# Kernel optimization log

Hardware: AMD Instinct MI355X
Metric: run time of the kernel (lower is better)

The kernel has to match this reference:

```python
import jax, jax.numpy as jnp
import numpy as np

N, H, O, E, K = 131072, 128, 128, 8, 2


def setup_inputs() -> dict:
    key = jax.random.key(0)
    k1, k2, k3, k4 = jax.random.split(key, 4)
    x = jax.random.normal(k1, (N, H), dtype=jnp.float32)
    w_gate = jax.random.normal(k2, (H, E), dtype=jnp.float32) * 0.02
    w_noise = jax.random.normal(k3, (H, E), dtype=jnp.float32) * 0.02
    w_expert = jax.random.normal(k4, (E, H, O), dtype=jnp.float32) * (1.0 / np.sqrt(H))
    b_expert = jnp.zeros((E, O), dtype=jnp.float32)
    return {"x": x, "w_gate": w_gate, "w_noise": w_noise,
            "w_expert": w_expert, "b_expert": b_expert, "top_k": K}


def _gates(x, w_gate, top_k):
    # Noisy top-k gating (eval mode: noise term w_noise is inactive).
    logits = x @ w_gate                              # [N, E]
    top_vals, top_idx = jax.lax.top_k(logits, top_k)  # [N, K]
    top_gates = jax.nn.softmax(top_vals, axis=-1)     # renormalize over top-k
    n = logits.shape[0]
    rows = jnp.arange(n)[:, None]                     # [N, 1]
    gates = jnp.zeros_like(logits).at[rows, top_idx].set(top_gates)  # [N, E] sparse
    return gates


def reference(x, w_gate, w_noise, w_expert, b_expert, top_k):
    gates = _gates(x, w_gate, top_k)                                  # [N, E]
    # Dense (mathematically identical) dispatch/combine: every expert FFN
    # applied per token, weighted by its (mostly-zero) gate.
    expert_out = jnp.einsum('nh,eho->neo', x, w_expert) + b_expert     # [N, E, O]
    out = jnp.einsum('ne,neo->no', gates, expert_out)                  # [N, O]
    return out
```

## Files before the change

### kernel.cpp

```cpp
#include <hip/hip_runtime.h>
#include <math.h>

typedef __bf16 bf16x8 __attribute__((ext_vector_type(8)));
typedef float f32x16 __attribute__((ext_vector_type(16)));

#define NTOK 131072
#define HDIM 128
#define ODIM 128
#define NEXP 8

__device__ __forceinline__ unsigned short f2bf(float f){
  union { float f; unsigned u; } v; v.f = f;
  unsigned r = v.u + 0x7FFFu + ((v.u >> 16) & 1u);
  return (unsigned short)(r >> 16);
}

__global__ void pack_w(const float* __restrict__ we, unsigned short* __restrict__ pw){
  int f = blockIdx.x * 256 + threadIdx.x;
  int l   = f & 63;
  int kt2 = (f >> 6) & 3;
  int e   = (f >> 8) & 7;
  int h   = (f >> 11) & 1;
  int ot  = (f >> 12) & 3;
  int o = ot * 32 + (l & 31);
  int kbase = (h * 4 + kt2) * 16 + ((l >> 5) << 3);
  unsigned short vals[8];
#pragma unroll
  for (int j = 0; j < 8; ++j)
    vals[j] = f2bf(we[(e * HDIM + kbase + j) * ODIM + o]);
  *(bf16x8*)(pw + (size_t)f * 8) = *(bf16x8*)vals;
}

__global__ void gating_pack(const float* __restrict__ x, const float* __restrict__ wg,
                            float* __restrict__ gates_t, unsigned short* __restrict__ xf){
  __shared__ float xs[64 * 128];
  __shared__ float wgl[128 * 8];
  __shared__ float plg[64 * 36];
  int t = threadIdx.x;
  size_t tokbase = (size_t)blockIdx.x * 64;

  ((float4*)wgl)[t] = ((const float4*)wg)[t];
  {
    const float4* xsrc = (const float4*)(x + tokbase * HDIM);
#pragma unroll
    for (int i = 0; i < 8; ++i){
      int idx = i * 256 + t;
      int tok = idx >> 5, c = idx & 31;
      *(float4*)&xs[tok * 128 + ((c ^ (tok & 7)) << 2)] = xsrc[idx];
    }
  }
  __syncthreads();

  {
    int tok = t & 63, q = t >> 6;
    float lg[8];
#pragma unroll
    for (int e = 0; e < 8; ++e) lg[e] = 0.0f;
#pragma unroll
    for (int i = 0; i < 8; ++i){
      int c = q * 8 + i;
      float4 v = *(float4*)&xs[tok * 128 + ((c ^ (tok & 7)) << 2)];
      const float* wr = wgl + c * 32;
#pragma unroll
      for (int e = 0; e < 8; ++e)
        lg[e] += v.x * wr[e] + v.y * wr[8 + e] + v.z * wr[16 + e] + v.w * wr[24 + e];
    }
    *(float4*)&plg[tok * 36 + q * 8]     = make_float4(lg[0], lg[1], lg[2], lg[3]);
    *(float4*)&plg[tok * 36 + q * 8 + 4] = make_float4(lg[4], lg[5], lg[6], lg[7]);
  }
  __syncthreads();

  if (t < 64){
    float lg[8];
#pragma unroll
    for (int e = 0; e < 8; ++e)
      lg[e] = plg[t * 36 + e] + plg[t * 36 + 8 + e] + plg[t * 36 + 16 + e] + plg[t * 36 + 24 + e];
    int i1 = 0; float v1 = lg[0];
#pragma unroll
    for (int e = 1; e < 8; ++e) if (lg[e] > v1){ v1 = lg[e]; i1 = e; }
    int i2 = -1; float v2 = -3.4e38f;
#pragma unroll
    for (int e = 0; e < 8; ++e) if (e != i1 && lg[e] > v2){ v2 = lg[e]; i2 = e; }
    float ex = __expf(v2 - v1);
    float inv = 1.0f / (1.0f + ex);
#pragma unroll
    for (int e = 0; e < 8; ++e)
      gates_t[(size_t)e * NTOK + tokbase + t] = (e == i1) ? inv : ((e == i2) ? ex * inv : 0.0f);
  }

  {
    int tokL = t >> 2, q = t & 3;
    float4 cv[8];
#pragma unroll
    for (int i = 0; i < 8; ++i)
      cv[i] = *(float4*)&xs[tokL * 128 + (((q * 8 + i) ^ (tokL & 7)) << 2)];
    size_t tgG = (size_t)blockIdx.x * 2 + (tokL >> 5);
#pragma unroll
    for (int jb = 0; jb < 4; ++jb){
      int h0 = q * 32 + jb * 8;
      int kt = h0 >> 4;
      int lslot = (tokL & 31) + 32 * (jb & 1);
      float4 a = cv[2 * jb], b = cv[2 * jb + 1];
      unsigned long long lo = (unsigned long long)f2bf(a.x)
                            | ((unsigned long long)f2bf(a.y) << 16)
                            | ((unsigned long long)f2bf(a.z) << 32)
                            | ((unsigned long long)f2bf(a.w) << 48);
      unsigned long long hi = (unsigned long long)f2bf(b.x)
                            | ((unsigned long long)f2bf(b.y) << 16)
                            | ((unsigned long long)f2bf(b.z) << 32)
                            | ((unsigned long long)f2bf(b.w) << 48);
      unsigned long long* dst = (unsigned long long*)(xf + ((tgG * 8 + kt) * 64 + lslot) * 8);
      dst[0] = lo; dst[1] = hi;
    }
  }
}

__launch_bounds__(256, 2)
__global__ void moe_gemm(const unsigned short* __restrict__ pw,
                         const unsigned short* __restrict__ xf,
                         const float* __restrict__ gates_t,
                         const float* __restrict__ be, float* __restrict__ out){
  __shared__ unsigned short Wh[16384];
  __shared__ float glds[8 * 512];
  __shared__ float blds[256];

  int t = threadIdx.x;
  int ot = blockIdx.x & 3;
  int tb = blockIdx.x >> 2;
  int w = t >> 6, l = t & 63, l32 = l & 31, lh = l >> 5;
  size_t tokb = (size_t)tb * 512;

#pragma unroll
  for (int it = 0; it < 4; ++it){
    int idx = it * 256 + t;
    int e = idx >> 7, c = idx & 127;
    *(float4*)&glds[e * 512 + c * 4] =
      *(const float4*)&gates_t[(size_t)e * NTOK + tokb + c * 4];
  }
  blds[t] = be[(t >> 5) * ODIM + ot * 32 + (t & 31)];

  f32x16 zero16;
#pragma unroll
  for (int i = 0; i < 16; ++i) zero16[i] = 0.0f;
  f32x16 tot0 = zero16, tot1 = zero16, tot2 = zero16, tot3 = zero16;

#pragma unroll 1
  for (int h = 0; h < 2; ++h){
    {
      const uint4* wsrc = (const uint4*)(pw + (size_t)(ot * 2 + h) * 16384);
      uint4* wdst = (uint4*)Wh;
#pragma unroll
      for (int it = 0; it < 8; ++it)
        wdst[it * 256 + t] = wsrc[it * 256 + t];
    }
    bf16x8 xb[4][4];
#pragma unroll
    for (int tg = 0; tg < 4; ++tg){
      size_t tgG = tokb / 32 + w * 4 + tg;
#pragma unroll
      for (int kt = 0; kt < 4; ++kt)
        xb[tg][kt] = *(const bf16x8*)(xf + ((tgG * 8 + h * 4 + kt) * 64 + l) * 8);
    }
    __syncthreads();

#pragma unroll 1
    for (int e = 0; e < 8; ++e){
      float g0 = glds[e * 512 + (w * 4 + 0) * 32 + l32];
      float g1 = glds[e * 512 + (w * 4 + 1) * 32 + l32];
      float g2 = glds[e * 512 + (w * 4 + 2) * 32 + l32];
      float g3 = glds[e * 512 + (w * 4 + 3) * 32 + l32];
      {
        f32x16 p0 = zero16, p1 = zero16;
#pragma unroll
        for (int kt = 0; kt < 4; ++kt){
          bf16x8 a = *(const bf16x8*)&Wh[((e * 4 + kt) * 64 + l) * 8];
          p0 = __builtin_amdgcn_mfma_f32_32x32x16_bf16(a, xb[0][kt], p0, 0, 0, 0);
          p1 = __builtin_amdgcn_mfma_f32_32x32x16_bf16(a, xb[1][kt], p1, 0, 0, 0);
        }
#pragma unroll
        for (int r = 0; r < 16; ++r){ tot0[r] += g0 * p0[r]; tot1[r] += g1 * p1[r]; }
      }
      {
        f32x16 p0 = zero16, p1 = zero16;
#pragma unroll
        for (int kt = 0; kt < 4; ++kt){
          bf16x8 a = *(const bf16x8*)&Wh[((e * 4 + kt) * 64 + l) * 8];
          p0 = __builtin_amdgcn_mfma_f32_32x32x16_bf16(a, xb[2][kt], p0, 0, 0, 0);
          p1 = __builtin_amdgcn_mfma_f32_32x32x16_bf16(a, xb[3][kt], p1, 0, 0, 0);
        }
#pragma unroll
        for (int r = 0; r < 16; ++r){ tot2[r] += g2 * p0[r]; tot3[r] += g3 * p1[r]; }
      }
    }
    __syncthreads();
  }

#pragma unroll
  for (int e = 0; e < 8; ++e){
    float bb[16];
#pragma unroll
    for (int rg = 0; rg < 4; ++rg){
      float4 b4 = *(float4*)&blds[e * 32 + rg * 8 + lh * 4];
      bb[rg * 4 + 0] = b4.x; bb[rg * 4 + 1] = b4.y; bb[rg * 4 + 2] = b4.z; bb[rg * 4 + 3] = b4.w;
    }
    float g0 = glds[e * 512 + (w * 4 + 0) * 32 + l32];
    float g1 = glds[e * 512 + (w * 4 + 1) * 32 + l32];
    float g2 = glds[e * 512 + (w * 4 + 2) * 32 + l32];
    float g3 = glds[e * 512 + (w * 4 + 3) * 32 + l32];
#pragma unroll
    for (int r = 0; r < 16; ++r){
      tot0[r] += g0 * bb[r]; tot1[r] += g1 * bb[r];
      tot2[r] += g2 * bb[r]; tot3[r] += g3 * bb[r];
    }
  }
#define STORE_TG(tg, tot)                                                       \
  {                                                                             \
    float* orow = out + (tokb + (size_t)(w * 4 + tg) * 32 + l32) * ODIM + ot * 32; \
    _Pragma("unroll")                                                           \
    for (int rg = 0; rg < 4; ++rg)                                              \
      *(float4*)(orow + rg * 8 + lh * 4) =                                      \
        make_float4(tot[rg * 4 + 0], tot[rg * 4 + 1], tot[rg * 4 + 2], tot[rg * 4 + 3]); \
  }
  STORE_TG(0, tot0) STORE_TG(1, tot1) STORE_TG(2, tot2) STORE_TG(3, tot3)
#undef STORE_TG
}

extern "C" void kernel_launch(void* const* d_in, const int* in_sizes, int n_in,
                              void* d_out, int out_size, void* d_ws, size_t ws_size,
                              hipStream_t stream){
  const float* x  = (const float*)d_in[0];
  const float* wg = (const float*)d_in[1];
  const float* we = (const float*)d_in[3];
  const float* be = (const float*)d_in[4];
  float* out = (float*)d_out;

  unsigned short* pw      = (unsigned short*)d_ws;
  float*          gates_t = (float*)((char*)d_ws + 262144);
  unsigned short* xf      = (unsigned short*)((char*)d_ws + 4456448);

  pack_w     <<<64,   256, 0, stream>>>(we, pw);
  gating_pack<<<2048, 256, 0, stream>>>(x, wg, gates_t, xf);
  moe_gemm   <<<1024, 256, 0, stream>>>(pw, xf, gates_t, be, out);
}
```

Measured before the change: 165.7 us.

## Halve tokens per moe_gemm block and read gates directly from global

Each moe_gemm block now covers 256 tokens instead of 512, with two 32-token groups per wave instead of four, and the grid doubles to 2048 blocks. Launch bounds rise to 4 blocks per SM. The shared-memory gate staging is removed; gates are loaded per expert straight from global memory. The aim is to cut register and LDS pressure so more blocks stay resident and hide latency, at the cost of staging the expert weight tile into LDS twice as often overall and issuing more scattered gate loads.

```diff
diff --git a/kernel.cpp b/kernel.cpp
--- a/kernel.cpp
+++ b/kernel.cpp
@@ -115,34 +115,26 @@
   }
 }
 
-__launch_bounds__(256, 2)
+__launch_bounds__(256, 4)
 __global__ void moe_gemm(const unsigned short* __restrict__ pw,
                          const unsigned short* __restrict__ xf,
                          const float* __restrict__ gates_t,
                          const float* __restrict__ be, float* __restrict__ out){
   __shared__ unsigned short Wh[16384];
-  __shared__ float glds[8 * 512];
   __shared__ float blds[256];
 
   int t = threadIdx.x;
   int ot = blockIdx.x & 3;
   int tb = blockIdx.x >> 2;
   int w = t >> 6, l = t & 63, l32 = l & 31, lh = l >> 5;
-  size_t tokb = (size_t)tb * 512;
-
-#pragma unroll
-  for (int it = 0; it < 4; ++it){
-    int idx = it * 256 + t;
-    int e = idx >> 7, c = idx & 127;
-    *(float4*)&glds[e * 512 + c * 4] =
-      *(const float4*)&gates_t[(size_t)e * NTOK + tokb + c * 4];
-  }
+  size_t tokb = (size_t)tb * 256;
+
   blds[t] = be[(t >> 5) * ODIM + ot * 32 + (t & 31)];
 
   f32x16 zero16;
 #pragma unroll
   for (int i = 0; i < 16; ++i) zero16[i] = 0.0f;
-  f32x16 tot0 = zero16, tot1 = zero16, tot2 = zero16, tot3 = zero16;
+  f32x16 tot0 = zero16, tot1 = zero16;
 
 #pragma unroll 1
   for (int h = 0; h < 2; ++h){
@@ -153,76 +145,58 @@
       for (int it = 0; it < 8; ++it)
         wdst[it * 256 + t] = wsrc[it * 256 + t];
     }
-    bf16x8 xb[4][4];
-#pragma unroll
-    for (int tg = 0; tg < 4; ++tg){
-      size_t tgG = tokb / 32 + w * 4 + tg;
-#pragma unroll
-      for (int kt = 0; kt < 4; ++kt)
-        xb[tg][kt] = *(const bf16x8*)(xf + ((tgG * 8 + h * 4 + kt) * 64 + l) * 8);
+    bf16x8 xb0[4], xb1[4];
+    {
+      size_t tgG = tokb / 32 + w * 2;
+#pragma unroll
+      for (int kt = 0; kt < 4; ++kt){
+        xb0[kt] = *(const bf16x8*)(xf + (((tgG + 0) * 8 + h * 4 + kt) * 64 + l) * 8);
+        xb1[kt] = *(const bf16x8*)(xf + (((tgG + 1) * 8 + h * 4 + kt) * 64 + l) * 8);
+      }
     }
     __syncthreads();
 
 #pragma unroll 1
     for (int e = 0; e < 8; ++e){
-      float g0 = glds[e * 512 + (w * 4 + 0) * 32 + l32];
-      float g1 = glds[e * 512 + (w * 4 + 1) * 32 + l32];
-      float g2 = glds[e * 512 + (w * 4 + 2) * 32 + l32];
-      float g3 = glds[e * 512 + (w * 4 + 3) * 32 + l32];
-      {
-        f32x16 p0 = zero16, p1 = zero16;
-#pragma unroll
-        for (int kt = 0; kt < 4; ++kt){
-          bf16x8 a = *(const bf16x8*)&Wh[((e * 4 + kt) * 64 + l) * 8];
-          p0 = __builtin_amdgcn_mfma_f32_32x32x16_bf16(a, xb[0][kt], p0, 0, 0, 0);
-          p1 = __builtin_amdgcn_mfma_f32_32x32x16_bf16(a, xb[1][kt], p1, 0, 0, 0);
-        }
-#pragma unroll
-        for (int r = 0; r < 16; ++r){ tot0[r] += g0 * p0[r]; tot1[r] += g1 * p1[r]; }
+      float g0 = gates_t[(size_t)e * NTOK + tokb + (w * 2 + 0) * 32 + l32];
+      float g1 = gates_t[(size_t)e * NTOK + tokb + (w * 2 + 1) * 32 + l32];
+      f32x16 p0 = zero16, p1 = zero16;
+#pragma unroll
+      for (int kt = 0; kt < 4; ++kt){
+        bf16x8 a = *(const bf16x8*)&Wh[((e * 4 + kt) * 64 + l) * 8];
+        p0 = __builtin_amdgcn_mfma_f32_32x32x16_bf16(a, xb0[kt], p0, 0, 0, 0);
+        p1 = __builtin_amdgcn_mfma_f32_32x32x16_bf16(a, xb1[kt], p1, 0, 0, 0);
       }
-      {
-        f32x16 p0 = zero16, p1 = zero16;
-#pragma unroll
-        for (int kt = 0; kt < 4; ++kt){
-          bf16x8 a = *(const bf16x8*)&Wh[((e * 4 + kt) * 64 + l) * 8];
-          p0 = __builtin_amdgcn_mfma_f32_32x32x16_bf16(a, xb[2][kt], p0, 0, 0, 0);
-          p1 = __builtin_amdgcn_mfma_f32_32x32x16_bf16(a, xb[3][kt], p1, 0, 0, 0);
-        }
-#pragma unroll
-        for (int r = 0; r < 16; ++r){ tot2[r] += g2 * p0[r]; tot3[r] += g3 * p1[r]; }
-      }
+#pragma unroll
+      for (int r = 0; r < 16; ++r){ tot0[r] += g0 * p0[r]; tot1[r] += g1 * p1[r]; }
     }
     __syncthreads();
   }
 
 #pragma unroll
   for (int e = 0; e < 8; ++e){
-    float bb[16];
+    float g0 = gates_t[(size_t)e * NTOK + tokb + (w * 2 + 0) * 32 + l32];
+    float g1 = gates_t[(size_t)e * NTOK + tokb + (w * 2 + 1) * 32 + l32];
 #pragma unroll
     for (int rg = 0; rg < 4; ++rg){
       float4 b4 = *(float4*)&blds[e * 32 + rg * 8 + lh * 4];
-      bb[rg * 4 + 0] = b4.x; bb[rg * 4 + 1] = b4.y; bb[rg * 4 + 2] = b4.z; bb[rg * 4 + 3] = b4.w;
-    }
-    float g0 = glds[e * 512 + (w * 4 + 0) * 32 + l32];
-    float g1 = glds[e * 512 + (w * 4 + 1) * 32 + l32];
-    float g2 = glds[e * 512 + (w * 4 + 2) * 32 + l32];
-    float g3 = glds[e * 512 + (w * 4 + 3) * 32 + l32];
-#pragma unroll
-    for (int r = 0; r < 16; ++r){
-      tot0[r] += g0 * bb[r]; tot1[r] += g1 * bb[r];
-      tot2[r] += g2 * bb[r]; tot3[r] += g3 * bb[r];
-    }
-  }
-#define STORE_TG(tg, tot)                                                       \
-  {                                                                             \
-    float* orow = out + (tokb + (size_t)(w * 4 + tg) * 32 + l32) * ODIM + ot * 32; \
-    _Pragma("unroll")                                                           \
-    for (int rg = 0; rg < 4; ++rg)                                              \
-      *(float4*)(orow + rg * 8 + lh * 4) =                                      \
-        make_float4(tot[rg * 4 + 0], tot[rg * 4 + 1], tot[rg * 4 + 2], tot[rg * 4 + 3]); \
-  }
-  STORE_TG(0, tot0) STORE_TG(1, tot1) STORE_TG(2, tot2) STORE_TG(3, tot3)
-#undef STORE_TG
+      tot0[rg * 4 + 0] += g0 * b4.x; tot0[rg * 4 + 1] += g0 * b4.y;
+      tot0[rg * 4 + 2] += g0 * b4.z; tot0[rg * 4 + 3] += g0 * b4.w;
+      tot1[rg * 4 + 0] += g1 * b4.x; tot1[rg * 4 + 1] += g1 * b4.y;
+      tot1[rg * 4 + 2] += g1 * b4.z; tot1[rg * 4 + 3] += g1 * b4.w;
+    }
+  }
+  {
+    float* orow0 = out + (tokb + (size_t)(w * 2 + 0) * 32 + l32) * ODIM + ot * 32;
+    float* orow1 = out + (tokb + (size_t)(w * 2 + 1) * 32 + l32) * ODIM + ot * 32;
+#pragma unroll
+    for (int rg = 0; rg < 4; ++rg){
+      *(float4*)(orow0 + rg * 8 + lh * 4) =
+        make_float4(tot0[rg * 4 + 0], tot0[rg * 4 + 1], tot0[rg * 4 + 2], tot0[rg * 4 + 3]);
+      *(float4*)(orow1 + rg * 8 + lh * 4) =
+        make_float4(tot1[rg * 4 + 0], tot1[rg * 4 + 1], tot1[rg * 4 + 2], tot1[rg * 4 + 3]);
+    }
+  }
 }
 
 extern "C" void kernel_launch(void* const* d_in, const int* in_sizes, int n_in,
@@ -240,5 +214,5 @@
 
   pack_w     <<<64,   256, 0, stream>>>(we, pw);
   gating_pack<<<2048, 256, 0, stream>>>(x, wg, gates_t, xf);
-  moe_gemm   <<<1024, 256, 0, stream>>>(pw, xf, gates_t, be, out);
-}
+  moe_gemm   <<<2048, 256, 0, stream>>>(pw, xf, gates_t, be, out);
+}
```

Result: no change. 165.8 us (+0.1%).
